# Performance work log

Hardware: AMD Instinct MI355X
Metric: run time of the kernel (lower is better)

The kernel has to match this reference:

```python
import jax, jax.numpy as jnp
import numpy as np

N = 50000      # nodes
E = 800000     # edges (before self loops)
IN = 256       # in_channels
HID = 64       # hidden_channels
HEADS = 2
NEG_SLOPE = 0.2
BN_EPS = 1e-5


def setup_inputs() -> dict:
    key = jax.random.key(0)
    ks = jax.random.split(key, 16)
    def g(i, shape, scale=0.05):
        return jax.random.normal(ks[i], shape, dtype=jnp.float32) * scale
    return {
        "x": jax.random.normal(ks[0], (N, IN), dtype=jnp.float32),
        "edge_index": jax.random.randint(ks[1], (2, E), 0, N, dtype=jnp.int64).astype(jnp.int32),
        # conv1 (GATv2, heads=2, concat)
        "W1l": g(2, (IN, HEADS * HID)), "b1l": jnp.zeros(HEADS * HID, jnp.float32),
        "W1r": g(3, (IN, HEADS * HID)), "b1r": jnp.zeros(HEADS * HID, jnp.float32),
        "att1": g(4, (HEADS, HID)), "bias1": jnp.zeros(HEADS * HID, jnp.float32),
        "bn1_g": jnp.ones(HEADS * HID, jnp.float32), "bn1_b": jnp.zeros(HEADS * HID, jnp.float32),
        "bn1_m": jnp.zeros(HEADS * HID, jnp.float32), "bn1_v": jnp.ones(HEADS * HID, jnp.float32),
        # conv2 (GATv2, heads=1)
        "W2l": g(5, (HEADS * HID, HID)), "b2l": jnp.zeros(HID, jnp.float32),
        "W2r": g(6, (HEADS * HID, HID)), "b2r": jnp.zeros(HID, jnp.float32),
        "att2": g(7, (1, HID)), "bias2": jnp.zeros(HID, jnp.float32),
        "bn2_g": jnp.ones(HID, jnp.float32), "bn2_b": jnp.zeros(HID, jnp.float32),
        "bn2_m": jnp.zeros(HID, jnp.float32), "bn2_v": jnp.ones(HID, jnp.float32),
        # classifier
        "Wc": g(8, (HID, 1)), "bc": jnp.zeros(1, jnp.float32),
    }


def _gatv2(x, src, dst, Wl, bl, Wr, br, att, bias, heads, ch, n):
    # GATv2: e_ij = att . leaky_relu(Wl x_j + Wr x_i); segment softmax over dst; out_i = sum alpha_ij Wl x_j
    xl = (x @ Wl + bl).reshape(n, heads, ch)  # source transform [N,H,C]
    xr = (x @ Wr + br).reshape(n, heads, ch)  # target transform [N,H,C]
    e = jax.nn.leaky_relu(xl[src] + xr[dst], NEG_SLOPE)        # [E,H,C]
    logits = jnp.einsum('ehc,hc->eh', e, att)                  # [E,H]
    m = jax.ops.segment_max(logits, dst, num_segments=n)       # [N,H]
    p = jnp.exp(logits - m[dst])
    s = jax.ops.segment_sum(p, dst, num_segments=n)            # [N,H]
    alpha = p / s[dst]                                         # [E,H]
    out = jax.ops.segment_sum(alpha[:, :, None] * xl[src], dst, num_segments=n)  # [N,H,C]
    return out.reshape(n, heads * ch) + bias


def _bn(x, g, b, m, v):
    return (x - m) * jax.lax.rsqrt(v + BN_EPS) * g + b


def reference(x, edge_index, W1l, b1l, W1r, b1r, att1, bias1,
              bn1_g, bn1_b, bn1_m, bn1_v,
              W2l, b2l, W2r, b2r, att2, bias2,
              bn2_g, bn2_b, bn2_m, bn2_v, Wc, bc):
    n = x.shape[0]
    loop = jnp.arange(n, dtype=edge_index.dtype)  # add_self_loops=True
    src = jnp.concatenate([edge_index[0], loop])
    dst = jnp.concatenate([edge_index[1], loop])
    h = _gatv2(x, src, dst, W1l, b1l, W1r, b1r, att1, bias1, HEADS, HID, n)
    h = jax.nn.elu(_bn(h, bn1_g, bn1_b, bn1_m, bn1_v))
    h = _gatv2(h, src, dst, W2l, b2l, W2r, b2r, att2, bias2, 1, HID, n)
    h = jax.nn.elu(_bn(h, bn2_g, bn2_b, bn2_m, bn2_v))
    return jax.nn.sigmoid(h @ Wc + bc)
```

## Files before the change

### kernel.cpp

```cpp
#include <hip/hip_runtime.h>
#include <hip/hip_bf16.h>
#include <cstddef>

#define NN 50000
#define EE 800000
#define TE 850000
#define INC 256
#define C1 128
#define C2 64
#define NCHUNK 49

typedef unsigned short ushort_t;
typedef short bf16x8 __attribute__((ext_vector_type(8)));
typedef float f32x4 __attribute__((ext_vector_type(4)));

__device__ inline ushort_t bf16r(float f) {
    unsigned u = __float_as_uint(f);
    unsigned r = (u + 0x7fffu + ((u >> 16) & 1u)) >> 16;
    return (ushort_t)r;
}
#define LOF(u) (__uint_as_float((u) << 16))
#define HIF(u) (__uint_as_float((u) & 0xffff0000u))
#define LRELU(t) (fmaxf((t), 0.f) + 0.2f * fminf((t), 0.f))
#define ELU(t) ((t) > 0.f ? (t) : (__expf(t) - 1.f))


__global__ void k_zero(int* p, int n) {
    int i = blockIdx.x * blockDim.x + threadIdx.x;
    if (i < n) p[i] = 0;
}

__global__ void k_count(const int* __restrict__ ei, int* __restrict__ deg,
                        int* __restrict__ rank) {
    int e = blockIdx.x * blockDim.x + threadIdx.x;
    if (e >= TE) return;
    int dst = (e < EE) ? ei[EE + e] : (e - EE);
    rank[e] = atomicAdd(&deg[dst], 1);
}

__global__ void k_scan1(const int* __restrict__ deg, int* __restrict__ incl,
                        int* __restrict__ totals) {
    __shared__ int lds[1024];
    int t = threadIdx.x;
    int i = blockIdx.x * 1024 + t;
    int v = (i < NN) ? deg[i] : 0;
    lds[t] = v;
    __syncthreads();
    for (int off = 1; off < 1024; off <<= 1) {
        int add = (t >= off) ? lds[t - off] : 0;
        __syncthreads();
        lds[t] += add;
        __syncthreads();
    }
    if (i < NN) incl[i] = lds[t];
    if (t == 1023) totals[blockIdx.x] = lds[t];
}

__global__ void k_scan2(const int* __restrict__ totals, int* __restrict__ chunkoff) {
    int t = threadIdx.x;
    int orig = (t < NCHUNK) ? totals[t] : 0;
    int v = orig;
    for (int off = 1; off < 64; off <<= 1) {
        int u = __shfl_up(v, off, 64);
        if (t >= off) v += u;
    }
    if (t < NCHUNK) chunkoff[t] = v - orig;
}

__global__ void k_scan3(const int* __restrict__ incl, const int* __restrict__ deg,
                        const int* __restrict__ chunkoff, int* __restrict__ rowstart) {
    int i = blockIdx.x * blockDim.x + threadIdx.x;
    if (i == 0) rowstart[NN] = TE;
    if (i >= NN) return;
    rowstart[i] = incl[i] - deg[i] + chunkoff[i >> 10];
}

__global__ void k_scatter(const int* __restrict__ ei, const int* __restrict__ rank,
                          const int* __restrict__ rowstart, int* __restrict__ ssrc) {
    int e = blockIdx.x * blockDim.x + threadIdx.x;
    if (e >= TE) return;
    int s, d;
    if (e < EE) { s = ei[e]; d = ei[EE + e]; }
    else        { s = e - EE; d = s; }
    ssrc[rowstart[d] + rank[e]] = s;
}


__global__ void k_cast4(const float* __restrict__ src, ushort_t* __restrict__ dst, int n4) {
    int i = blockIdx.x * blockDim.x + threadIdx.x;
    if (i >= n4) return;
    float4 a = ((const float4*)src)[i];
    ushort4 o;
    o.x = bf16r(a.x); o.y = bf16r(a.y); o.z = bf16r(a.z); o.w = bf16r(a.w);
    ((ushort4*)dst)[i] = o;
}

__global__ void k_prep_w(const float* __restrict__ Wl, const float* __restrict__ Wr,
                         const float* __restrict__ bl, const float* __restrict__ br,
                         ushort_t* __restrict__ Wt, float* __restrict__ biasf,
                         int K, int HALF) {
    int n = blockIdx.x;
    int k = threadIdx.x;
    const float* W = (n < HALF) ? Wl : Wr;
    int c = (n < HALF) ? n : n - HALF;
    Wt[(size_t)n * K + k] = bf16r(W[(size_t)k * HALF + c]);
    if (n == 0 && k < 2 * HALF) biasf[k] = (k < HALF) ? bl[k] : br[k - HALF];
}


template <int K, int NCOL>
__global__ __launch_bounds__(256) void k_gemm_mfma(const ushort_t* __restrict__ A,
                                                   const ushort_t* __restrict__ Bt,
                                                   const float* __restrict__ bias,
                                                   ushort_t* __restrict__ C, int M) {
    __shared__ __align__(16) ushort_t As[128 * 40];
    __shared__ __align__(16) ushort_t Bs[128 * 40];
    int tid = threadIdx.x;
    int bm = blockIdx.x * 128;
    int bn = blockIdx.y * 128;
    int w = tid >> 6, l = tid & 63;
    int wm = (w & 1) * 64, wn = (w >> 1) * 64;
    int lm = l & 15, half = l >> 4;

    f32x4 zero = {0.f, 0.f, 0.f, 0.f};
    f32x4 acc[4][4];
#pragma unroll
    for (int a = 0; a < 4; a++)
#pragma unroll
        for (int b = 0; b < 4; b++) acc[a][b] = zero;

    for (int k0 = 0; k0 < K; k0 += 32) {
#pragma unroll
        for (int q = 0; q < 2; q++) {
            int seg = q * 256 + tid;
            int m = seg >> 2;
            int ko = (seg & 3) * 8;
            *(float4*)&As[m * 40 + ko] = *(const float4*)&A[(size_t)(bm + m) * K + k0 + ko];
            *(float4*)&Bs[m * 40 + ko] = *(const float4*)&Bt[(size_t)(bn + m) * K + k0 + ko];
        }
        __syncthreads();
        bf16x8 af[4], bfr[4];
#pragma unroll
        for (int mi = 0; mi < 4; mi++)
            af[mi] = *(const bf16x8*)&As[(wm + mi * 16 + lm) * 40 + half * 8];
#pragma unroll
        for (int ni = 0; ni < 4; ni++)
            bfr[ni] = *(const bf16x8*)&Bs[(wn + ni * 16 + lm) * 40 + half * 8];
#pragma unroll
        for (int mi = 0; mi < 4; mi++)
#pragma unroll
            for (int ni = 0; ni < 4; ni++)
                acc[mi][ni] = __builtin_amdgcn_mfma_f32_16x16x32_bf16(
                    af[mi], bfr[ni], acc[mi][ni], 0, 0, 0);
        __syncthreads();
    }
#pragma unroll
    for (int ni = 0; ni < 4; ni++) {
        int col = bn + wn + ni * 16 + lm;
        float bv = bias[col];
#pragma unroll
        for (int mi = 0; mi < 4; mi++) {
            int rbase = bm + wm + mi * 16 + half * 4;
#pragma unroll
            for (int r = 0; r < 4; r++) {
                int row = rbase + r;
                if (row < M) C[(size_t)row * NCOL + col] = bf16r(acc[mi][ni][r] + bv);
            }
        }
    }
}


__global__ __launch_bounds__(256) void k_fused1(
    const ushort_t* __restrict__ xlr, const int* __restrict__ rowstart,
    const int* __restrict__ ssrc, const float* __restrict__ att,
    const float* __restrict__ bias,
    const float* __restrict__ g, const float* __restrict__ b,
    const float* __restrict__ m, const float* __restrict__ v,
    ushort_t* __restrict__ out) {
    int lane = threadIdx.x & 63;
    int i = blockIdx.x * 4 + (threadIdx.x >> 6);
    if (i >= NN) return;
    int hw = lane >> 5;
    int c2 = lane & 31;
    uint2 xru = *(const uint2*)&xlr[(size_t)i * 256 + 128 + 4 * c2];
    float xr0 = LOF(xru.x), xr1 = HIF(xru.x), xr2 = LOF(xru.y), xr3 = HIF(xru.y);
    float4 at = *(const float4*)&att[4 * c2];
    int row = rowstart[i], end = rowstart[i + 1];
    float a0 = 0.f, a1 = 0.f, a2 = 0.f, a3 = 0.f, s = 0.f;
    int j = row;
    for (; j + 8 <= end; j += 8) {
        int src[4];
        uint2 u[4];
#pragma unroll
        for (int k = 0; k < 4; k++) src[k] = ssrc[j + 2 * k + hw];
#pragma unroll
        for (int k = 0; k < 4; k++)
            u[k] = *(const uint2*)&xlr[(size_t)src[k] * 256 + 4 * c2];
        float d[4], f0[4], f1[4], f2[4], f3[4];
#pragma unroll
        for (int k = 0; k < 4; k++) {
            f0[k] = LOF(u[k].x); f1[k] = HIF(u[k].x);
            f2[k] = LOF(u[k].y); f3[k] = HIF(u[k].y);
            float t0 = f0[k] + xr0, t1 = f1[k] + xr1;
            float t2 = f2[k] + xr2, t3 = f3[k] + xr3;
            d[k] = at.x * LRELU(t0) + at.y * LRELU(t1)
                 + at.z * LRELU(t2) + at.w * LRELU(t3);
        }
#pragma unroll
        for (int o = 1; o <= 8; o <<= 1) {
#pragma unroll
            for (int k = 0; k < 4; k++) d[k] += __shfl_xor(d[k], o, 64);
        }
#pragma unroll
        for (int k = 0; k < 4; k++) {
            float p = __expf(d[k]);
            a0 += p * f0[k]; a1 += p * f1[k];
            a2 += p * f2[k]; a3 += p * f3[k];
            s += p;
        }
    }
    for (; j < end; j += 2) {
        int je = j + hw;
        bool valid = je < end;
        int src = valid ? ssrc[je] : i;
        uint2 uu = *(const uint2*)&xlr[(size_t)src * 256 + 4 * c2];
        float f0 = LOF(uu.x), f1 = HIF(uu.x), f2 = LOF(uu.y), f3 = HIF(uu.y);
        float t0 = f0 + xr0, t1 = f1 + xr1, t2 = f2 + xr2, t3 = f3 + xr3;
        float d = at.x * LRELU(t0) + at.y * LRELU(t1)
                + at.z * LRELU(t2) + at.w * LRELU(t3);
        d += __shfl_xor(d, 1, 64);
        d += __shfl_xor(d, 2, 64);
        d += __shfl_xor(d, 4, 64);
        d += __shfl_xor(d, 8, 64);
        float p = valid ? __expf(d) : 0.f;
        a0 += p * f0; a1 += p * f1; a2 += p * f2; a3 += p * f3;
        s += p;
    }
    a0 += __shfl_xor(a0, 32, 64);
    a1 += __shfl_xor(a1, 32, 64);
    a2 += __shfl_xor(a2, 32, 64);
    a3 += __shfl_xor(a3, 32, 64);
    s  += __shfl_xor(s, 32, 64);
    if (hw == 0) {
        float inv = 1.f / s;
        float4 bb = *(const float4*)&bias[4 * c2];
        float4 mm = *(const float4*)&m[4 * c2];
        float4 vv = *(const float4*)&v[4 * c2];
        float4 gg = *(const float4*)&g[4 * c2];
        float4 b2 = *(const float4*)&b[4 * c2];
        float o0 = a0 * inv + bb.x, o1 = a1 * inv + bb.y;
        float o2 = a2 * inv + bb.z, o3 = a3 * inv + bb.w;
        o0 = (o0 - mm.x) * rsqrtf(vv.x + 1e-5f) * gg.x + b2.x;
        o1 = (o1 - mm.y) * rsqrtf(vv.y + 1e-5f) * gg.y + b2.y;
        o2 = (o2 - mm.z) * rsqrtf(vv.z + 1e-5f) * gg.z + b2.z;
        o3 = (o3 - mm.w) * rsqrtf(vv.w + 1e-5f) * gg.w + b2.w;
        o0 = ELU(o0); o1 = ELU(o1); o2 = ELU(o2); o3 = ELU(o3);
        uint2 wp;
        wp.x = (unsigned)bf16r(o0) | ((unsigned)bf16r(o1) << 16);
        wp.y = (unsigned)bf16r(o2) | ((unsigned)bf16r(o3) << 16);
        *(uint2*)&out[(size_t)i * C1 + 4 * c2] = wp;
    }
}

__global__ __launch_bounds__(256) void k_fused2(
    const ushort_t* __restrict__ xlr, const int* __restrict__ rowstart,
    const int* __restrict__ ssrc, const float* __restrict__ att,
    const float* __restrict__ bias,
    const float* __restrict__ g, const float* __restrict__ b,
    const float* __restrict__ m, const float* __restrict__ v,
    const float* __restrict__ Wc, const float* __restrict__ bc,
    float* __restrict__ out) {
    int lane = threadIdx.x & 63;
    int i = blockIdx.x * 4 + (threadIdx.x >> 6);
    if (i >= NN) return;
    int qw = lane >> 4;
    int c4 = lane & 15;
    uint2 xru = *(const uint2*)&xlr[(size_t)i * 128 + 64 + 4 * c4];
    float xr0 = LOF(xru.x), xr1 = HIF(xru.x), xr2 = LOF(xru.y), xr3 = HIF(xru.y);
    float4 at = *(const float4*)&att[4 * c4];
    int row = rowstart[i], end = rowstart[i + 1];
    float a0 = 0.f, a1 = 0.f, a2 = 0.f, a3 = 0.f, s = 0.f;
    int j = row;
    for (; j + 8 <= end; j += 8) {
        int src[2];
        uint2 u[2];
#pragma unroll
        for (int k = 0; k < 2; k++) src[k] = ssrc[j + 4 * k + qw];
#pragma unroll
        for (int k = 0; k < 2; k++)
            u[k] = *(const uint2*)&xlr[(size_t)src[k] * 128 + 4 * c4];
        float d[2], f0[2], f1[2], f2[2], f3[2];
#pragma unroll
        for (int k = 0; k < 2; k++) {
            f0[k] = LOF(u[k].x); f1[k] = HIF(u[k].x);
            f2[k] = LOF(u[k].y); f3[k] = HIF(u[k].y);
            float t0 = f0[k] + xr0, t1 = f1[k] + xr1;
            float t2 = f2[k] + xr2, t3 = f3[k] + xr3;
            d[k] = at.x * LRELU(t0) + at.y * LRELU(t1)
                 + at.z * LRELU(t2) + at.w * LRELU(t3);
        }
#pragma unroll
        for (int o = 1; o <= 8; o <<= 1) {
#pragma unroll
            for (int k = 0; k < 2; k++) d[k] += __shfl_xor(d[k], o, 64);
        }
#pragma unroll
        for (int k = 0; k < 2; k++) {
            float p = __expf(d[k]);
            a0 += p * f0[k]; a1 += p * f1[k];
            a2 += p * f2[k]; a3 += p * f3[k];
            s += p;
        }
    }
    for (; j < end; j += 4) {
        int je = j + qw;
        bool valid = je < end;
        int src = valid ? ssrc[je] : i;
        uint2 uu = *(const uint2*)&xlr[(size_t)src * 128 + 4 * c4];
        float f0 = LOF(uu.x), f1 = HIF(uu.x), f2 = LOF(uu.y), f3 = HIF(uu.y);
        float t0 = f0 + xr0, t1 = f1 + xr1, t2 = f2 + xr2, t3 = f3 + xr3;
        float d = at.x * LRELU(t0) + at.y * LRELU(t1)
                + at.z * LRELU(t2) + at.w * LRELU(t3);
        d += __shfl_xor(d, 1, 64);
        d += __shfl_xor(d, 2, 64);
        d += __shfl_xor(d, 4, 64);
        d += __shfl_xor(d, 8, 64);
        float p = valid ? __expf(d) : 0.f;
        a0 += p * f0; a1 += p * f1; a2 += p * f2; a3 += p * f3;
        s += p;
    }
#pragma unroll
    for (int o = 16; o <= 32; o <<= 1) {
        a0 += __shfl_xor(a0, o, 64);
        a1 += __shfl_xor(a1, o, 64);
        a2 += __shfl_xor(a2, o, 64);
        a3 += __shfl_xor(a3, o, 64);
        s  += __shfl_xor(s, o, 64);
    }
    float inv = 1.f / s;
    float4 bb = *(const float4*)&bias[4 * c4];
    float4 mm = *(const float4*)&m[4 * c4];
    float4 vv = *(const float4*)&v[4 * c4];
    float4 gg = *(const float4*)&g[4 * c4];
    float4 b2 = *(const float4*)&b[4 * c4];
    float o0 = a0 * inv + bb.x, o1 = a1 * inv + bb.y;
    float o2 = a2 * inv + bb.z, o3 = a3 * inv + bb.w;
    o0 = (o0 - mm.x) * rsqrtf(vv.x + 1e-5f) * gg.x + b2.x;
    o1 = (o1 - mm.y) * rsqrtf(vv.y + 1e-5f) * gg.y + b2.y;
    o2 = (o2 - mm.z) * rsqrtf(vv.z + 1e-5f) * gg.z + b2.z;
    o3 = (o3 - mm.w) * rsqrtf(vv.w + 1e-5f) * gg.w + b2.w;
    o0 = ELU(o0); o1 = ELU(o1); o2 = ELU(o2); o3 = ELU(o3);
    float4 wc = *(const float4*)&Wc[4 * c4];
    float z = o0 * wc.x + o1 * wc.y + o2 * wc.z + o3 * wc.w;
    z += __shfl_xor(z, 1, 64);
    z += __shfl_xor(z, 2, 64);
    z += __shfl_xor(z, 4, 64);
    z += __shfl_xor(z, 8, 64);
    if (lane == 0) out[i] = 1.f / (1.f + __expf(-(z + bc[0])));
}


extern "C" void kernel_launch(void* const* d_in, const int* in_sizes, int n_in,
                              void* d_out, int out_size, void* d_ws, size_t ws_size,
                              hipStream_t stream) {
    const float* x    = (const float*)d_in[0];
    const int*   ei   = (const int*)d_in[1];
    const float* W1l  = (const float*)d_in[2];
    const float* b1l  = (const float*)d_in[3];
    const float* W1r  = (const float*)d_in[4];
    const float* b1r  = (const float*)d_in[5];
    const float* att1 = (const float*)d_in[6];
    const float* bias1= (const float*)d_in[7];
    const float* bn1g = (const float*)d_in[8];
    const float* bn1b = (const float*)d_in[9];
    const float* bn1m = (const float*)d_in[10];
    const float* bn1v = (const float*)d_in[11];
    const float* W2l  = (const float*)d_in[12];
    const float* b2l  = (const float*)d_in[13];
    const float* W2r  = (const float*)d_in[14];
    const float* b2r  = (const float*)d_in[15];
    const float* att2 = (const float*)d_in[16];
    const float* bias2= (const float*)d_in[17];
    const float* bn2g = (const float*)d_in[18];
    const float* bn2b = (const float*)d_in[19];
    const float* bn2m = (const float*)d_in[20];
    const float* bn2v = (const float*)d_in[21];
    const float* Wc   = (const float*)d_in[22];
    const float* bc   = (const float*)d_in[23];
    float* out = (float*)d_out;

    char* ws = (char*)d_ws;
    size_t off = 0;
    auto alloc = [&](size_t bytes) {
        size_t o = off;
        off += (bytes + 255) & ~(size_t)255;
        return o;
    };
    ushort_t* xb    = (ushort_t*)(ws + alloc((size_t)(NN + 128) * 256 * 2));
    ushort_t* xlr1  = (ushort_t*)(ws + alloc((size_t)NN * 256 * 2));
    ushort_t* h1b   = (ushort_t*)(ws + alloc((size_t)(NN + 128) * 128 * 2));
    ushort_t* Wt1   = (ushort_t*)(ws + alloc((size_t)256 * 256 * 2));
    float*    biasf1= (float*)(ws + alloc(256 * 4));
    ushort_t* Wt2   = (ushort_t*)(ws + alloc((size_t)128 * 128 * 2));
    float*    biasf2= (float*)(ws + alloc(128 * 4));
    int* deg      = (int*)(ws + alloc((size_t)NN * 4));
    int* incl     = (int*)(ws + alloc((size_t)NN * 4));
    int* rowstart = (int*)(ws + alloc((size_t)(NN + 1) * 4));
    int* totals   = (int*)(ws + alloc(64 * 4));
    int* chunkoff = (int*)(ws + alloc(64 * 4));
    int* rank     = (int*)(ws + alloc((size_t)TE * 4));
    int* ssrc     = (int*)(ws + alloc((size_t)TE * 4));
    ushort_t* xlr2 = xlr1;

    k_zero<<<(NN + 255) / 256, 256, 0, stream>>>(deg, NN);
    k_count<<<(TE + 255) / 256, 256, 0, stream>>>(ei, deg, rank);
    k_scan1<<<NCHUNK, 1024, 0, stream>>>(deg, incl, totals);
    k_scan2<<<1, 64, 0, stream>>>(totals, chunkoff);
    k_scan3<<<(NN + 255) / 256, 256, 0, stream>>>(incl, deg, chunkoff, rowstart);
    k_scatter<<<(TE + 255) / 256, 256, 0, stream>>>(ei, rank, rowstart, ssrc);

    int n4x = NN * INC / 4;
    k_cast4<<<(n4x + 255) / 256, 256, 0, stream>>>(x, xb, n4x);
    k_prep_w<<<256, 256, 0, stream>>>(W1l, W1r, b1l, b1r, Wt1, biasf1, 256, 128);
    k_prep_w<<<128, 128, 0, stream>>>(W2l, W2r, b2l, b2r, Wt2, biasf2, 128, 64);

    dim3 gg1((NN + 127) / 128, 2);
    k_gemm_mfma<256, 256><<<gg1, 256, 0, stream>>>(xb, Wt1, biasf1, xlr1, NN);
    k_fused1<<<(NN + 3) / 4, 256, 0, stream>>>(xlr1, rowstart, ssrc, att1, bias1,
                                               bn1g, bn1b, bn1m, bn1v, h1b);

    dim3 gg2((NN + 127) / 128, 1);
    k_gemm_mfma<128, 128><<<gg2, 256, 0, stream>>>(h1b, Wt2, biasf2, xlr2, NN);
    k_fused2<<<(NN + 3) / 4, 256, 0, stream>>>(xlr2, rowstart, ssrc, att2, bias2,
                                               bn2g, bn2b, bn2m, bn2v, Wc, bc, out);
}
```

Measured before the change: 322.4 us.

## Merge independent preprocessing kernels into multi-role launches to cut launch count

Combines edge counting, input cast and both weight transposes into one kernel whose blocks pick their role by block index. The CSR scatter is folded into the first GEMM launch as extra blocks, and the zeroing kernel becomes a memset. The aim is fewer kernel launches and fewer launch gaps, with independent work running side by side on the GPU. The cost is larger mixed grids, and the scatter blocks may be held back behind GEMM blocks that use more LDS.

Result: faster. 307.2 us (-4.7%).

```diff
diff --git a/kernel.cpp b/kernel.cpp
--- a/kernel.cpp
+++ b/kernel.cpp
@@ -10,6 +10,14 @@
 #define C2 64
 #define NCHUNK 49
 
+#define NB_COUNT 3321
+#define NB_CAST  12500
+#define NB_P1    256
+#define NB_P2    128
+#define NB_K1    (NB_COUNT + NB_CAST + NB_P1 + NB_P2)
+#define NB_GEMM1 782
+#define NB_K2    (NB_GEMM1 + NB_COUNT)
+
 typedef unsigned short ushort_t;
 typedef short bf16x8 __attribute__((ext_vector_type(8)));
 typedef float f32x4 __attribute__((ext_vector_type(4)));
@@ -24,19 +32,6 @@
 #define LRELU(t) (fmaxf((t), 0.f) + 0.2f * fminf((t), 0.f))
 #define ELU(t) ((t) > 0.f ? (t) : (__expf(t) - 1.f))
 
-
-__global__ void k_zero(int* p, int n) {
-    int i = blockIdx.x * blockDim.x + threadIdx.x;
-    if (i < n) p[i] = 0;
-}
-
-__global__ void k_count(const int* __restrict__ ei, int* __restrict__ deg,
-                        int* __restrict__ rank) {
-    int e = blockIdx.x * blockDim.x + threadIdx.x;
-    if (e >= TE) return;
-    int dst = (e < EE) ? ei[EE + e] : (e - EE);
-    rank[e] = atomicAdd(&deg[dst], 1);
-}
 
 __global__ void k_scan1(const int* __restrict__ deg, int* __restrict__ incl,
                         int* __restrict__ totals) {
@@ -75,49 +70,57 @@
     rowstart[i] = incl[i] - deg[i] + chunkoff[i >> 10];
 }
 
-__global__ void k_scatter(const int* __restrict__ ei, const int* __restrict__ rank,
-                          const int* __restrict__ rowstart, int* __restrict__ ssrc) {
-    int e = blockIdx.x * blockDim.x + threadIdx.x;
-    if (e >= TE) return;
-    int s, d;
-    if (e < EE) { s = ei[e]; d = ei[EE + e]; }
-    else        { s = e - EE; d = s; }
-    ssrc[rowstart[d] + rank[e]] = s;
-}
-
-
-__global__ void k_cast4(const float* __restrict__ src, ushort_t* __restrict__ dst, int n4) {
-    int i = blockIdx.x * blockDim.x + threadIdx.x;
-    if (i >= n4) return;
-    float4 a = ((const float4*)src)[i];
-    ushort4 o;
-    o.x = bf16r(a.x); o.y = bf16r(a.y); o.z = bf16r(a.z); o.w = bf16r(a.w);
-    ((ushort4*)dst)[i] = o;
-}
-
-__global__ void k_prep_w(const float* __restrict__ Wl, const float* __restrict__ Wr,
-                         const float* __restrict__ bl, const float* __restrict__ br,
-                         ushort_t* __restrict__ Wt, float* __restrict__ biasf,
-                         int K, int HALF) {
-    int n = blockIdx.x;
-    int k = threadIdx.x;
-    const float* W = (n < HALF) ? Wl : Wr;
-    int c = (n < HALF) ? n : n - HALF;
-    Wt[(size_t)n * K + k] = bf16r(W[(size_t)k * HALF + c]);
-    if (n == 0 && k < 2 * HALF) biasf[k] = (k < HALF) ? bl[k] : br[k - HALF];
+
+__global__ __launch_bounds__(256) void k_stage1(
+    const int* __restrict__ ei, int* __restrict__ deg, int* __restrict__ rank,
+    const float* __restrict__ x, ushort_t* __restrict__ xb,
+    const float* __restrict__ W1l, const float* __restrict__ W1r,
+    const float* __restrict__ b1l, const float* __restrict__ b1r,
+    ushort_t* __restrict__ Wt1, float* __restrict__ biasf1,
+    const float* __restrict__ W2l, const float* __restrict__ W2r,
+    const float* __restrict__ b2l, const float* __restrict__ b2r,
+    ushort_t* __restrict__ Wt2, float* __restrict__ biasf2) {
+    int b = blockIdx.x;
+    int tid = threadIdx.x;
+    if (b < NB_COUNT) {
+        int e = b * 256 + tid;
+        if (e < TE) {
+            int dst = (e < EE) ? ei[EE + e] : (e - EE);
+            rank[e] = atomicAdd(&deg[dst], 1);
+        }
+    } else if (b < NB_COUNT + NB_CAST) {
+        int i = (b - NB_COUNT) * 256 + tid;
+        float4 a = ((const float4*)x)[i];
+        ushort4 o;
+        o.x = bf16r(a.x); o.y = bf16r(a.y); o.z = bf16r(a.z); o.w = bf16r(a.w);
+        ((ushort4*)xb)[i] = o;
+    } else if (b < NB_COUNT + NB_CAST + NB_P1) {
+        int n = b - NB_COUNT - NB_CAST;
+        int k = tid;
+        const float* W = (n < 128) ? W1l : W1r;
+        int c = (n < 128) ? n : n - 128;
+        Wt1[(size_t)n * 256 + k] = bf16r(W[(size_t)k * 128 + c]);
+        if (n == 0) biasf1[k] = (k < 128) ? b1l[k] : b1r[k - 128];
+    } else {
+        int n = b - NB_COUNT - NB_CAST - NB_P1;
+        int k = tid;
+        if (k < 128) {
+            const float* W = (n < 64) ? W2l : W2r;
+            int c = (n < 64) ? n : n - 64;
+            Wt2[(size_t)n * 128 + k] = bf16r(W[(size_t)k * 64 + c]);
+            if (n == 0) biasf2[k] = (k < 64) ? b2l[k] : b2r[k - 64];
+        }
+    }
 }
 
 
 template <int K, int NCOL>
-__global__ __launch_bounds__(256) void k_gemm_mfma(const ushort_t* __restrict__ A,
-                                                   const ushort_t* __restrict__ Bt,
-                                                   const float* __restrict__ bias,
-                                                   ushort_t* __restrict__ C, int M) {
-    __shared__ __align__(16) ushort_t As[128 * 40];
-    __shared__ __align__(16) ushort_t Bs[128 * 40];
+__device__ inline void gemm_body(const ushort_t* __restrict__ A,
+                                 const ushort_t* __restrict__ Bt,
+                                 const float* __restrict__ bias,
+                                 ushort_t* __restrict__ C, int M,
+                                 int bm, int bn, ushort_t* As, ushort_t* Bs) {
     int tid = threadIdx.x;
-    int bm = blockIdx.x * 128;
-    int bn = blockIdx.y * 128;
     int w = tid >> 6, l = tid & 63;
     int wm = (w & 1) * 64, wn = (w >> 1) * 64;
     int lm = l & 15, half = l >> 4;
@@ -168,6 +171,39 @@
             }
         }
     }
+}
+
+
+__global__ __launch_bounds__(256) void k_gemm1_scatter(
+    const ushort_t* __restrict__ A, const ushort_t* __restrict__ Bt,
+    const float* __restrict__ bias, ushort_t* __restrict__ C,
+    const int* __restrict__ ei, const int* __restrict__ rank,
+    const int* __restrict__ rowstart, int* __restrict__ ssrc) {
+    __shared__ __align__(16) ushort_t As[128 * 40];
+    __shared__ __align__(16) ushort_t Bs[128 * 40];
+    int b = blockIdx.x;
+    if (b < NB_GEMM1) {
+        int bm = (b >> 1) * 128;
+        int bn = (b & 1) * 128;
+        gemm_body<256, 256>(A, Bt, bias, C, NN, bm, bn, As, Bs);
+    } else {
+        int e = (b - NB_GEMM1) * 256 + threadIdx.x;
+        if (e < TE) {
+            int s, d;
+            if (e < EE) { s = ei[e]; d = ei[EE + e]; }
+            else        { s = e - EE; d = s; }
+            ssrc[rowstart[d] + rank[e]] = s;
+        }
+    }
+}
+
+__global__ __launch_bounds__(256) void k_gemm2(
+    const ushort_t* __restrict__ A, const ushort_t* __restrict__ Bt,
+    const float* __restrict__ bias, ushort_t* __restrict__ C) {
+    __shared__ __align__(16) ushort_t As[128 * 40];
+    __shared__ __align__(16) ushort_t Bs[128 * 40];
+    int bm = blockIdx.x * 128;
+    gemm_body<128, 128>(A, Bt, bias, C, NN, bm, 0, As, Bs);
 }
 
 
@@ -413,25 +449,23 @@
     int* ssrc     = (int*)(ws + alloc((size_t)TE * 4));
     ushort_t* xlr2 = xlr1;
 
-    k_zero<<<(NN + 255) / 256, 256, 0, stream>>>(deg, NN);
-    k_count<<<(TE + 255) / 256, 256, 0, stream>>>(ei, deg, rank);
+    hipMemsetAsync(deg, 0, (size_t)NN * 4, stream);
+
+    k_stage1<<<NB_K1, 256, 0, stream>>>(ei, deg, rank, x, xb,
+                                        W1l, W1r, b1l, b1r, Wt1, biasf1,
+                                        W2l, W2r, b2l, b2r, Wt2, biasf2);
+
     k_scan1<<<NCHUNK, 1024, 0, stream>>>(deg, incl, totals);
     k_scan2<<<1, 64, 0, stream>>>(totals, chunkoff);
     k_scan3<<<(NN + 255) / 256, 256, 0, stream>>>(incl, deg, chunkoff, rowstart);
-    k_scatter<<<(TE + 255) / 256, 256, 0, stream>>>(ei, rank, rowstart, ssrc);
-
-    int n4x = NN * INC / 4;
-    k_cast4<<<(n4x + 255) / 256, 256, 0, stream>>>(x, xb, n4x);
-    k_prep_w<<<256, 256, 0, stream>>>(W1l, W1r, b1l, b1r, Wt1, biasf1, 256, 128);
-    k_prep_w<<<128, 128, 0, stream>>>(W2l, W2r, b2l, b2r, Wt2, biasf2, 128, 64);
-
-    dim3 gg1((NN + 127) / 128, 2);
-    k_gemm_mfma<256, 256><<<gg1, 256, 0, stream>>>(xb, Wt1, biasf1, xlr1, NN);
+
+    k_gemm1_scatter<<<NB_K2, 256, 0, stream>>>(xb, Wt1, biasf1, xlr1,
+                                               ei, rank, rowstart, ssrc);
+
     k_fused1<<<(NN + 3) / 4, 256, 0, stream>>>(xlr1, rowstart, ssrc, att1, bias1,
                                                bn1g, bn1b, bn1m, bn1v, h1b);
 
-    dim3 gg2((NN + 127) / 128, 1);
-    k_gemm_mfma<128, 128><<<gg2, 256, 0, stream>>>(h1b, Wt2, biasf2, xlr2, NN);
+    k_gemm2<<<(NN + 127) / 128, 256, 0, stream>>>(h1b, Wt2, biasf2, xlr2);
     k_fused2<<<(NN + 3) / 4, 256, 0, stream>>>(xlr2, rowstart, ssrc, att2, bias2,
                                                bn2g, bn2b, bn2m, bn2v, Wc, bc, out);
 }
```
